# Kernel optimization log

Hardware: AMD Instinct MI355X
Metric: run time of the kernel (lower is better)

Reference implementation:

```python
import jax, jax.numpy as jnp
import numpy as np

N, E, C, H = 50000, 1_600_000, 128, 128
NUM_GRAPHS = 64


def setup_inputs() -> dict:
    key = jax.random.key(0)
    ks = jax.random.split(key, 9)
    x = jax.random.normal(ks[0], (N, C), dtype=jnp.float32)
    edge_index = jax.random.randint(ks[1], (2, E), 0, N, dtype=jnp.int64)
    edge_index_neg = jax.random.randint(ks[2], (2, E), 0, N, dtype=jnp.int64)
    batch = jnp.sort(jax.random.randint(ks[3], (N,), 0, NUM_GRAPHS, dtype=jnp.int64))
    W1 = jax.random.normal(ks[4], (C, H), dtype=jnp.float32) * 0.05
    b1 = jnp.zeros((H,), dtype=jnp.float32)
    W2 = jax.random.normal(ks[5], (H, H), dtype=jnp.float32) * 0.05
    b2 = jnp.zeros((H,), dtype=jnp.float32)
    We = jax.random.normal(ks[6], (2 * H, 1), dtype=jnp.float32) * 0.05
    be = jnp.zeros((1,), dtype=jnp.float32)
    return {"x": x, "edge_index": edge_index, "edge_index_neg": edge_index_neg,
            "batch": batch, "W1": W1, "b1": b1, "W2": W2, "b2": b2,
            "We": We, "be": be}


def reference(x, edge_index, edge_index_neg, batch, W1, b1, W2, b2, We, be):
    # x_enc: Linear -> ReLU -> Linear, then outer ReLU activation (eval mode, dropout=0)
    h = jax.nn.relu(jnp.dot(x, W1) + b1)          # [N, H]
    h = jax.nn.relu(jnp.dot(h, W2) + b2)          # [N, H]
    # p_e_x(cat([q, k])) == q @ We[:H] + k @ We[H:] + be  (avoids materializing cat)
    hdim = W1.shape[1]
    Wq, Wk = We[:hdim], We[hdim:]                  # [H,1] each

    def edge_score(ei):
        q = h[ei[0]]                               # [E, H] gather
        k = h[ei[1]]                               # [E, H] gather
        return jnp.dot(q, Wq) + jnp.dot(k, Wk) + be  # [E, 1]

    e_pred_pos = edge_score(edge_index)
    e_pred_neg = edge_score(edge_index_neg)
    return (e_pred_pos, e_pred_neg, edge_index_neg)
```

## Files before the change

kernel.cpp:

```cpp
#include <hip/hip_runtime.h>

#define CDIM 128
#define HDIM 128
#define LIM  40960

typedef short bf16x8 __attribute__((ext_vector_type(8)));
typedef float f32x16 __attribute__((ext_vector_type(16)));

static __device__ __forceinline__ short f2bf(float f) {
    union { float f; unsigned u; } v; v.f = f;
    unsigned r = v.u + 0x7FFFu + ((v.u >> 16) & 1u);
    return (short)(r >> 16);
}
static __device__ __forceinline__ unsigned pack2(float a, float b) {
    return (unsigned)(unsigned short)f2bf(a) | ((unsigned)(unsigned short)f2bf(b) << 16);
}

__global__ __launch_bounds__(256) void prep_kernel(
    const float* __restrict__ W1, const float* __restrict__ W2,
    short* __restrict__ wf1, short* __restrict__ wf2)
{
    int id = blockIdx.x * 256 + threadIdx.x;
    const float* src = (id < 16384) ? W1 : W2;
    short* dst = (id < 16384) ? wf1 : wf2;
    int rem = id & 16383;
    int j  = rem & 7;
    int l  = (rem >> 3) & 63;
    int ks = (rem >> 9) & 7;
    int ct = rem >> 12;
    int k = ks * 16 + (l >> 5) * 8 + j;
    int n = ct * 32 + (l & 31);
    dst[rem] = f2bf(src[k * HDIM + n]);
}

__global__ __launch_bounds__(256, 2) void node_mfma(
    const float* __restrict__ x,
    const short* __restrict__ wf1, const float* __restrict__ b1,
    const short* __restrict__ wf2, const float* __restrict__ b2,
    const float* __restrict__ We,
    unsigned* __restrict__ tab, int N)
{
    __shared__ __align__(16) short wfA[2][16384];
    __shared__ __align__(16) float cv[512];

    const int tid = threadIdx.x;
    const int w   = tid >> 6;
    const int l   = tid & 63;
    const int col = l & 31;
    const int hi  = l >> 5;
    const int node = blockIdx.x * 128 + w * 32 + col;

#pragma unroll
    for (int t = 0; t < 16; t++) {
        int c = (t * 4 + w) * 64;
        const uint4* src = (c < 2048) ? ((const uint4*)wf1 + c)
                                      : ((const uint4*)wf2 + (c - 2048));
        __builtin_amdgcn_global_load_lds(
            (const __attribute__((address_space(1))) void*)(src + l),
            (__attribute__((address_space(3))) void*)((char*)wfA + (size_t)c * 16),
            16, 0, 0);
    }
    for (int i = tid; i < 512; i += 256)
        cv[i] = (i < 128) ? b1[i] : (i < 256) ? b2[i - 128] : We[i - 256];
    __syncthreads();

    const f32x16 zz = {0.f,0.f,0.f,0.f,0.f,0.f,0.f,0.f,0.f,0.f,0.f,0.f,0.f,0.f,0.f,0.f};

    const int nclamp = (node < N) ? node : (N - 1);
    const float* xb = &x[(size_t)nclamp * CDIM + hi * 8];
    f32x16 acc[4];
#pragma unroll
    for (int ct = 0; ct < 4; ct++) acc[ct] = zz;

#pragma unroll
    for (int ks = 0; ks < 8; ks++) {
        float4 v0 = *(const float4*)(xb + ks * 16);
        float4 v1 = *(const float4*)(xb + ks * 16 + 4);
        bf16x8 a;
        a[0] = f2bf(v0.x); a[1] = f2bf(v0.y); a[2] = f2bf(v0.z); a[3] = f2bf(v0.w);
        a[4] = f2bf(v1.x); a[5] = f2bf(v1.y); a[6] = f2bf(v1.z); a[7] = f2bf(v1.w);
#pragma unroll
        for (int ct = 0; ct < 4; ct++) {
            bf16x8 wfrag = *(const bf16x8*)&wfA[0][((ct * 8 + ks) * 64 + l) * 8];
            acc[ct] = __builtin_amdgcn_mfma_f32_32x32x16_bf16(wfrag, a, acc[ct], 0, 0, 0);
        }
    }

    unsigned P[4][4][2], Q[4][4][2];
#pragma unroll
    for (int ct = 0; ct < 4; ct++) {
#pragma unroll
        for (int g = 0; g < 4; g++) {
            float4 bv = *(const float4*)&cv[32 * ct + 8 * g + 4 * hi];
            float h0 = fmaxf(acc[ct][4 * g + 0] + bv.x, 0.f);
            float h1v = fmaxf(acc[ct][4 * g + 1] + bv.y, 0.f);
            float h2v = fmaxf(acc[ct][4 * g + 2] + bv.z, 0.f);
            float h3v = fmaxf(acc[ct][4 * g + 3] + bv.w, 0.f);
            P[ct][g][0] = pack2(h0, h1v);
            P[ct][g][1] = pack2(h2v, h3v);
        }
    }
#pragma unroll
    for (int ct = 0; ct < 4; ct++)
#pragma unroll
        for (int g = 0; g < 4; g++)
#pragma unroll
            for (int p = 0; p < 2; p++)
                Q[ct][g][p] = (unsigned)__shfl_xor((int)P[ct][g][p], 32, 64);

    f32x16 acc2[4];
#pragma unroll
    for (int ct = 0; ct < 4; ct++) acc2[ct] = zz;

#pragma unroll
    for (int ks2 = 0; ks2 < 8; ks2++) {
        const int c  = ks2 >> 1;
        const int s2 = (ks2 & 1) * 2;
        union { bf16x8 v; unsigned u[4]; } bb;
        bb.u[0] = hi ? Q[c][s2 + 1][0] : P[c][s2][0];
        bb.u[1] = hi ? Q[c][s2 + 1][1] : P[c][s2][1];
        bb.u[2] = hi ? P[c][s2 + 1][0] : Q[c][s2][0];
        bb.u[3] = hi ? P[c][s2 + 1][1] : Q[c][s2][1];
#pragma unroll
        for (int ct = 0; ct < 4; ct++) {
            bf16x8 wfrag = *(const bf16x8*)&wfA[1][((ct * 8 + ks2) * 64 + l) * 8];
            acc2[ct] = __builtin_amdgcn_mfma_f32_32x32x16_bf16(wfrag, bb.v, acc2[ct], 0, 0, 0);
        }
    }

    float pq = 0.f, pk = 0.f;
#pragma unroll
    for (int ct = 0; ct < 4; ct++) {
#pragma unroll
        for (int g = 0; g < 4; g++) {
            float4 b2v = *(const float4*)&cv[128 + 32 * ct + 8 * g + 4 * hi];
            float4 wqv = *(const float4*)&cv[256 + 32 * ct + 8 * g + 4 * hi];
            float4 wkv = *(const float4*)&cv[384 + 32 * ct + 8 * g + 4 * hi];
            const float* b2a = (const float*)&b2v;
            const float* wqa = (const float*)&wqv;
            const float* wka = (const float*)&wkv;
#pragma unroll
            for (int i = 0; i < 4; i++) {
                float hv = fmaxf(acc2[ct][4 * g + i] + b2a[i], 0.f);
                pq = fmaf(hv, wqa[i], pq);
                pk = fmaf(hv, wka[i], pk);
            }
        }
    }
    pq += __shfl_xor(pq, 32, 64);
    pk += __shfl_xor(pk, 32, 64);
    if (hi == 0 && node < N) tab[node] = pack2(pq, pk);
}

__global__ __launch_bounds__(1024) void edge_kernel(
    const int* __restrict__ eip, const int* __restrict__ ein,
    const unsigned* __restrict__ tab, const float* __restrict__ be_p,
    float* __restrict__ out, int E)
{
    __shared__ __align__(16) unsigned lt[LIM];
    const int tid = threadIdx.x;
    const int wv = tid >> 6, ln = tid & 63;

    const uint4* tg4 = (const uint4*)tab;
#pragma unroll
    for (int t = 0; t < LIM / 4 / 1024; t++) {
        int c = (t * 16 + wv) * 64;
        __builtin_amdgcn_global_load_lds(
            (const __attribute__((address_space(1))) void*)(tg4 + c + ln),
            (__attribute__((address_space(3))) void*)((char*)lt + (size_t)c * 16),
            16, 0, 0);
    }
    __builtin_amdgcn_sched_barrier(0);

    const int U = E >> 2;
    const int chunk = (U + gridDim.x - 1) / gridDim.x;
    const int ustart = blockIdx.x * chunk;
    const int uend = min(U, ustart + chunk);

    const int4* eip4 = (const int4*)eip;
    const int4* ein4 = (const int4*)ein;
    float4* out4 = (float4*)out;

    const int u0 = ustart + tid, u1 = u0 + 1024;
    const bool v0 = u0 < uend, v1 = u1 < uend;
    int4 ns0 = {0,0,0,0}, nd0 = {0,0,0,0}, ns1 = {0,0,0,0}, nd1 = {0,0,0,0};
    if (v0) {
        ns0 = ein4[u0]; nd0 = ein4[U + u0];
        out4[2 * U + u0] = make_float4((float)ns0.x, (float)ns0.y, (float)ns0.z, (float)ns0.w);
        out4[3 * U + u0] = make_float4((float)nd0.x, (float)nd0.y, (float)nd0.z, (float)nd0.w);
    }
    if (v1) {
        ns1 = ein4[u1]; nd1 = ein4[U + u1];
        out4[2 * U + u1] = make_float4((float)ns1.x, (float)ns1.y, (float)ns1.z, (float)ns1.w);
        out4[3 * U + u1] = make_float4((float)nd1.x, (float)nd1.y, (float)nd1.z, (float)nd1.w);
    }
    __syncthreads();

    const float be = be_p[0];
#define GATHER(i) ((i) < LIM ? lt[i] : tab[i])
#define SCORE(us, ud) (__uint_as_float((us) << 16) + __uint_as_float((ud) & 0xFFFF0000u) + be)

    if (v0) {
        int4 ps = eip4[u0], pd = eip4[U + u0];
        unsigned a0 = GATHER(ps.x), a1 = GATHER(ps.y), a2 = GATHER(ps.z), a3 = GATHER(ps.w);
        unsigned b0 = GATHER(pd.x), b1 = GATHER(pd.y), b2 = GATHER(pd.z), b3 = GATHER(pd.w);
        unsigned c0 = GATHER(ns0.x), c1 = GATHER(ns0.y), c2 = GATHER(ns0.z), c3 = GATHER(ns0.w);
        unsigned d0 = GATHER(nd0.x), d1 = GATHER(nd0.y), d2 = GATHER(nd0.z), d3 = GATHER(nd0.w);
        out4[u0]     = make_float4(SCORE(a0,b0), SCORE(a1,b1), SCORE(a2,b2), SCORE(a3,b3));
        out4[U + u0] = make_float4(SCORE(c0,d0), SCORE(c1,d1), SCORE(c2,d2), SCORE(c3,d3));
    }
    if (v1) {
        int4 ps = eip4[u1], pd = eip4[U + u1];
        unsigned a0 = GATHER(ps.x), a1 = GATHER(ps.y), a2 = GATHER(ps.z), a3 = GATHER(ps.w);
        unsigned b0 = GATHER(pd.x), b1 = GATHER(pd.y), b2 = GATHER(pd.z), b3 = GATHER(pd.w);
        unsigned c0 = GATHER(ns1.x), c1 = GATHER(ns1.y), c2 = GATHER(ns1.z), c3 = GATHER(ns1.w);
        unsigned d0 = GATHER(nd1.x), d1 = GATHER(nd1.y), d2 = GATHER(nd1.z), d3 = GATHER(nd1.w);
        out4[u1]     = make_float4(SCORE(a0,b0), SCORE(a1,b1), SCORE(a2,b2), SCORE(a3,b3));
        out4[U + u1] = make_float4(SCORE(c0,d0), SCORE(c1,d1), SCORE(c2,d2), SCORE(c3,d3));
    }
#undef GATHER
#undef SCORE
}

extern "C" void kernel_launch(void* const* d_in, const int* in_sizes, int n_in,
                              void* d_out, int out_size, void* d_ws, size_t ws_size,
                              hipStream_t stream) {
    const float* x   = (const float*)d_in[0];
    const int*   eip = (const int*)d_in[1];
    const int*   ein = (const int*)d_in[2];
    const float* W1  = (const float*)d_in[4];
    const float* b1  = (const float*)d_in[5];
    const float* W2  = (const float*)d_in[6];
    const float* b2  = (const float*)d_in[7];
    const float* We  = (const float*)d_in[8];
    const float* be  = (const float*)d_in[9];

    const int N = in_sizes[0] / CDIM;
    const int E = in_sizes[1] / 2;

    char* ws = (char*)d_ws;
    unsigned* tab = (unsigned*)ws;
    short*    wf1 = (short*)(ws + 200704);
    short*    wf2 = (short*)(ws + 200704 + 32768);

    prep_kernel<<<128, 256, 0, stream>>>(W1, W2, wf1, wf2);
    node_mfma<<<(N + 127) / 128, 256, 0, stream>>>(x, wf1, b1, wf2, b2, We, tab, N);
    edge_kernel<<<256, 1024, 0, stream>>>(eip, ein, tab, be, (float*)d_out, E);
}
```

Measured before the change: 32.69 us.

## Move negative edge-index copy into node kernel and enlarge node tiles

The float cast of edge_index_neg into the output moves out of the edge kernel and into the node MLP kernel. That kernel now runs as a fixed grid of 256 blocks with 512 threads and 256 nodes per block; blocks past N only do the copy. The x loads are hoisted ahead of the weight-staging barrier, and the prep kernel now reads W1/W2 coalesced and scatters its writes. The edge kernel issues its index loads earlier. The aim is to spread the copy bandwidth over the compute-bound node phase and shorten the gather kernel, at the cost of more registers per thread in the node kernel.

```diff
diff --git a/kernel.cpp b/kernel.cpp
--- a/kernel.cpp
+++ b/kernel.cpp
@@ -2,6 +2,7 @@
 
 #define CDIM 128
 #define HDIM 128
+#define TILE 256
 #define LIM  40960
 
 typedef short bf16x8 __attribute__((ext_vector_type(8)));
@@ -24,21 +25,20 @@
     const float* src = (id < 16384) ? W1 : W2;
     short* dst = (id < 16384) ? wf1 : wf2;
     int rem = id & 16383;
-    int j  = rem & 7;
-    int l  = (rem >> 3) & 63;
-    int ks = (rem >> 9) & 7;
-    int ct = rem >> 12;
-    int k = ks * 16 + (l >> 5) * 8 + j;
-    int n = ct * 32 + (l & 31);
-    dst[rem] = f2bf(src[k * HDIM + n]);
-}
-
-__global__ __launch_bounds__(256, 2) void node_mfma(
+    int k = rem >> 7, n = rem & 127;
+    int ks = k >> 4, j = k & 7;
+    int l  = (n & 31) + 32 * ((k >> 3) & 1);
+    int ct = n >> 5;
+    dst[((ct * 8 + ks) * 64 + l) * 8 + j] = f2bf(src[rem]);
+}
+
+__global__ __launch_bounds__(512) void node_mfma(
     const float* __restrict__ x,
     const short* __restrict__ wf1, const float* __restrict__ b1,
     const short* __restrict__ wf2, const float* __restrict__ b2,
     const float* __restrict__ We,
-    unsigned* __restrict__ tab, int N)
+    const int* __restrict__ ein,
+    unsigned* __restrict__ tab, float* __restrict__ out, int N, int E)
 {
     __shared__ __align__(16) short wfA[2][16384];
     __shared__ __align__(16) float cv[512];
@@ -48,108 +48,127 @@
     const int l   = tid & 63;
     const int col = l & 31;
     const int hi  = l >> 5;
-    const int node = blockIdx.x * 128 + w * 32 + col;
-
-#pragma unroll
-    for (int t = 0; t < 16; t++) {
-        int c = (t * 4 + w) * 64;
-        const uint4* src = (c < 2048) ? ((const uint4*)wf1 + c)
-                                      : ((const uint4*)wf2 + (c - 2048));
-        __builtin_amdgcn_global_load_lds(
-            (const __attribute__((address_space(1))) void*)(src + l),
-            (__attribute__((address_space(3))) void*)((char*)wfA + (size_t)c * 16),
-            16, 0, 0);
-    }
-    for (int i = tid; i < 512; i += 256)
-        cv[i] = (i < 128) ? b1[i] : (i < 256) ? b2[i - 128] : We[i - 256];
-    __syncthreads();
-
-    const f32x16 zz = {0.f,0.f,0.f,0.f,0.f,0.f,0.f,0.f,0.f,0.f,0.f,0.f,0.f,0.f,0.f,0.f};
-
-    const int nclamp = (node < N) ? node : (N - 1);
-    const float* xb = &x[(size_t)nclamp * CDIM + hi * 8];
-    f32x16 acc[4];
-#pragma unroll
-    for (int ct = 0; ct < 4; ct++) acc[ct] = zz;
-
-#pragma unroll
-    for (int ks = 0; ks < 8; ks++) {
-        float4 v0 = *(const float4*)(xb + ks * 16);
-        float4 v1 = *(const float4*)(xb + ks * 16 + 4);
-        bf16x8 a;
-        a[0] = f2bf(v0.x); a[1] = f2bf(v0.y); a[2] = f2bf(v0.z); a[3] = f2bf(v0.w);
-        a[4] = f2bf(v1.x); a[5] = f2bf(v1.y); a[6] = f2bf(v1.z); a[7] = f2bf(v1.w);
+    const int node = blockIdx.x * TILE + w * 32 + col;
+    const bool nodeblk = (blockIdx.x * TILE) < N;
+
+    if (nodeblk) {
+#pragma unroll
+        for (int t = 0; t < 8; t++) {
+            int c = (t * 8 + w) * 64;
+            const uint4* src = (c < 2048) ? ((const uint4*)wf1 + c)
+                                          : ((const uint4*)wf2 + (c - 2048));
+            __builtin_amdgcn_global_load_lds(
+                (const __attribute__((address_space(1))) void*)(src + l),
+                (__attribute__((address_space(3))) void*)((char*)wfA + (size_t)c * 16),
+                16, 0, 0);
+        }
+        cv[tid] = (tid < 128) ? b1[tid] : (tid < 256) ? b2[tid - 128] : We[tid - 256];
+
+        const int nclamp = (node < N) ? node : (N - 1);
+        const float* xb = &x[(size_t)nclamp * CDIM + hi * 8];
+        bf16x8 af[8];
+#pragma unroll
+        for (int ks = 0; ks < 8; ks++) {
+            float4 v0 = *(const float4*)(xb + ks * 16);
+            float4 v1 = *(const float4*)(xb + ks * 16 + 4);
+            af[ks][0] = f2bf(v0.x); af[ks][1] = f2bf(v0.y);
+            af[ks][2] = f2bf(v0.z); af[ks][3] = f2bf(v0.w);
+            af[ks][4] = f2bf(v1.x); af[ks][5] = f2bf(v1.y);
+            af[ks][6] = f2bf(v1.z); af[ks][7] = f2bf(v1.w);
+        }
+        __syncthreads();
+
+        const f32x16 zz = {0.f,0.f,0.f,0.f,0.f,0.f,0.f,0.f,0.f,0.f,0.f,0.f,0.f,0.f,0.f,0.f};
+
+        f32x16 acc[4];
+#pragma unroll
+        for (int ct = 0; ct < 4; ct++) acc[ct] = zz;
+#pragma unroll
+        for (int ks = 0; ks < 8; ks++) {
+#pragma unroll
+            for (int ct = 0; ct < 4; ct++) {
+                bf16x8 wfrag = *(const bf16x8*)&wfA[0][((ct * 8 + ks) * 64 + l) * 8];
+                acc[ct] = __builtin_amdgcn_mfma_f32_32x32x16_bf16(wfrag, af[ks], acc[ct], 0, 0, 0);
+            }
+        }
+
+        unsigned P[4][4][2], Q[4][4][2];
 #pragma unroll
         for (int ct = 0; ct < 4; ct++) {
-            bf16x8 wfrag = *(const bf16x8*)&wfA[0][((ct * 8 + ks) * 64 + l) * 8];
-            acc[ct] = __builtin_amdgcn_mfma_f32_32x32x16_bf16(wfrag, a, acc[ct], 0, 0, 0);
-        }
-    }
-
-    unsigned P[4][4][2], Q[4][4][2];
-#pragma unroll
-    for (int ct = 0; ct < 4; ct++) {
-#pragma unroll
-        for (int g = 0; g < 4; g++) {
-            float4 bv = *(const float4*)&cv[32 * ct + 8 * g + 4 * hi];
-            float h0 = fmaxf(acc[ct][4 * g + 0] + bv.x, 0.f);
-            float h1v = fmaxf(acc[ct][4 * g + 1] + bv.y, 0.f);
-            float h2v = fmaxf(acc[ct][4 * g + 2] + bv.z, 0.f);
-            float h3v = fmaxf(acc[ct][4 * g + 3] + bv.w, 0.f);
-            P[ct][g][0] = pack2(h0, h1v);
-            P[ct][g][1] = pack2(h2v, h3v);
-        }
-    }
-#pragma unroll
-    for (int ct = 0; ct < 4; ct++)
-#pragma unroll
-        for (int g = 0; g < 4; g++)
-#pragma unroll
-            for (int p = 0; p < 2; p++)
-                Q[ct][g][p] = (unsigned)__shfl_xor((int)P[ct][g][p], 32, 64);
-
-    f32x16 acc2[4];
-#pragma unroll
-    for (int ct = 0; ct < 4; ct++) acc2[ct] = zz;
-
-#pragma unroll
-    for (int ks2 = 0; ks2 < 8; ks2++) {
-        const int c  = ks2 >> 1;
-        const int s2 = (ks2 & 1) * 2;
-        union { bf16x8 v; unsigned u[4]; } bb;
-        bb.u[0] = hi ? Q[c][s2 + 1][0] : P[c][s2][0];
-        bb.u[1] = hi ? Q[c][s2 + 1][1] : P[c][s2][1];
-        bb.u[2] = hi ? P[c][s2 + 1][0] : Q[c][s2][0];
-        bb.u[3] = hi ? P[c][s2 + 1][1] : Q[c][s2][1];
+#pragma unroll
+            for (int g = 0; g < 4; g++) {
+                float4 bv = *(const float4*)&cv[32 * ct + 8 * g + 4 * hi];
+                float h0  = fmaxf(acc[ct][4 * g + 0] + bv.x, 0.f);
+                float h1v = fmaxf(acc[ct][4 * g + 1] + bv.y, 0.f);
+                float h2v = fmaxf(acc[ct][4 * g + 2] + bv.z, 0.f);
+                float h3v = fmaxf(acc[ct][4 * g + 3] + bv.w, 0.f);
+                P[ct][g][0] = pack2(h0, h1v);
+                P[ct][g][1] = pack2(h2v, h3v);
+            }
+        }
+#pragma unroll
+        for (int ct = 0; ct < 4; ct++)
+#pragma unroll
+            for (int g = 0; g < 4; g++)
+#pragma unroll
+                for (int p = 0; p < 2; p++)
+                    Q[ct][g][p] = (unsigned)__shfl_xor((int)P[ct][g][p], 32, 64);
+
+        f32x16 acc2[4];
+#pragma unroll
+        for (int ct = 0; ct < 4; ct++) acc2[ct] = zz;
+#pragma unroll
+        for (int ks2 = 0; ks2 < 8; ks2++) {
+            const int c  = ks2 >> 1;
+            const int s2 = (ks2 & 1) * 2;
+            union { bf16x8 v; unsigned u[4]; } bb;
+            bb.u[0] = hi ? Q[c][s2 + 1][0] : P[c][s2][0];
+            bb.u[1] = hi ? Q[c][s2 + 1][1] : P[c][s2][1];
+            bb.u[2] = hi ? P[c][s2 + 1][0] : Q[c][s2][0];
+            bb.u[3] = hi ? P[c][s2 + 1][1] : Q[c][s2][1];
+#pragma unroll
+            for (int ct = 0; ct < 4; ct++) {
+                bf16x8 wfrag = *(const bf16x8*)&wfA[1][((ct * 8 + ks2) * 64 + l) * 8];
+                acc2[ct] = __builtin_amdgcn_mfma_f32_32x32x16_bf16(wfrag, bb.v, acc2[ct], 0, 0, 0);
+            }
+        }
+
+        float pq = 0.f, pk = 0.f;
 #pragma unroll
         for (int ct = 0; ct < 4; ct++) {
-            bf16x8 wfrag = *(const bf16x8*)&wfA[1][((ct * 8 + ks2) * 64 + l) * 8];
-            acc2[ct] = __builtin_amdgcn_mfma_f32_32x32x16_bf16(wfrag, bb.v, acc2[ct], 0, 0, 0);
-        }
-    }
-
-    float pq = 0.f, pk = 0.f;
-#pragma unroll
-    for (int ct = 0; ct < 4; ct++) {
-#pragma unroll
-        for (int g = 0; g < 4; g++) {
-            float4 b2v = *(const float4*)&cv[128 + 32 * ct + 8 * g + 4 * hi];
-            float4 wqv = *(const float4*)&cv[256 + 32 * ct + 8 * g + 4 * hi];
-            float4 wkv = *(const float4*)&cv[384 + 32 * ct + 8 * g + 4 * hi];
-            const float* b2a = (const float*)&b2v;
-            const float* wqa = (const float*)&wqv;
-            const float* wka = (const float*)&wkv;
-#pragma unroll
-            for (int i = 0; i < 4; i++) {
-                float hv = fmaxf(acc2[ct][4 * g + i] + b2a[i], 0.f);
-                pq = fmaf(hv, wqa[i], pq);
-                pk = fmaf(hv, wka[i], pk);
-            }
-        }
-    }
-    pq += __shfl_xor(pq, 32, 64);
-    pk += __shfl_xor(pk, 32, 64);
-    if (hi == 0 && node < N) tab[node] = pack2(pq, pk);
+#pragma unroll
+            for (int g = 0; g < 4; g++) {
+                float4 b2v = *(const float4*)&cv[128 + 32 * ct + 8 * g + 4 * hi];
+                float4 wqv = *(const float4*)&cv[256 + 32 * ct + 8 * g + 4 * hi];
+                float4 wkv = *(const float4*)&cv[384 + 32 * ct + 8 * g + 4 * hi];
+                const float* b2a = (const float*)&b2v;
+                const float* wqa = (const float*)&wqv;
+                const float* wka = (const float*)&wkv;
+#pragma unroll
+                for (int i = 0; i < 4; i++) {
+                    float hv = fmaxf(acc2[ct][4 * g + i] + b2a[i], 0.f);
+                    pq = fmaf(hv, wqa[i], pq);
+                    pk = fmaf(hv, wka[i], pk);
+                }
+            }
+        }
+        pq += __shfl_xor(pq, 32, 64);
+        pk += __shfl_xor(pk, 32, 64);
+        if (hi == 0 && node < N) tab[node] = pack2(pq, pk);
+    }
+
+    {
+        const int castU = (E * 2) >> 2;
+        const int chunk = (castU + gridDim.x - 1) / gridDim.x;
+        const int base = blockIdx.x * chunk;
+        const int lim = min(castU, base + chunk);
+        const int4* ein4 = (const int4*)ein;
+        float4* o4 = (float4*)out + (E >> 1);
+        for (int i = base + tid; i < lim; i += 512) {
+            int4 v = ein4[i];
+            o4[i] = make_float4((float)v.x, (float)v.y, (float)v.z, (float)v.w);
+        }
+    }
 }
 
 __global__ __launch_bounds__(1024) void edge_kernel(
@@ -183,39 +202,35 @@
 
     const int u0 = ustart + tid, u1 = u0 + 1024;
     const bool v0 = u0 < uend, v1 = u1 < uend;
+
     int4 ns0 = {0,0,0,0}, nd0 = {0,0,0,0}, ns1 = {0,0,0,0}, nd1 = {0,0,0,0};
+    int4 ps0 = {0,0,0,0}, pd0 = {0,0,0,0};
     if (v0) {
         ns0 = ein4[u0]; nd0 = ein4[U + u0];
-        out4[2 * U + u0] = make_float4((float)ns0.x, (float)ns0.y, (float)ns0.z, (float)ns0.w);
-        out4[3 * U + u0] = make_float4((float)nd0.x, (float)nd0.y, (float)nd0.z, (float)nd0.w);
-    }
-    if (v1) {
-        ns1 = ein4[u1]; nd1 = ein4[U + u1];
-        out4[2 * U + u1] = make_float4((float)ns1.x, (float)ns1.y, (float)ns1.z, (float)ns1.w);
-        out4[3 * U + u1] = make_float4((float)nd1.x, (float)nd1.y, (float)nd1.z, (float)nd1.w);
-    }
+        ps0 = eip4[u0]; pd0 = eip4[U + u0];
+    }
+    if (v1) { ns1 = ein4[u1]; nd1 = ein4[U + u1]; }
+
     __syncthreads();
 
     const float be = be_p[0];
 #define GATHER(i) ((i) < LIM ? lt[i] : tab[i])
 #define SCORE(us, ud) (__uint_as_float((us) << 16) + __uint_as_float((ud) & 0xFFFF0000u) + be)
-
     if (v0) {
-        int4 ps = eip4[u0], pd = eip4[U + u0];
-        unsigned a0 = GATHER(ps.x), a1 = GATHER(ps.y), a2 = GATHER(ps.z), a3 = GATHER(ps.w);
-        unsigned b0 = GATHER(pd.x), b1 = GATHER(pd.y), b2 = GATHER(pd.z), b3 = GATHER(pd.w);
+        unsigned a0 = GATHER(ps0.x), a1 = GATHER(ps0.y), a2 = GATHER(ps0.z), a3 = GATHER(ps0.w);
+        unsigned b0 = GATHER(pd0.x), b1 = GATHER(pd0.y), b2 = GATHER(pd0.z), b3 = GATHER(pd0.w);
+        out4[u0] = make_float4(SCORE(a0,b0), SCORE(a1,b1), SCORE(a2,b2), SCORE(a3,b3));
         unsigned c0 = GATHER(ns0.x), c1 = GATHER(ns0.y), c2 = GATHER(ns0.z), c3 = GATHER(ns0.w);
         unsigned d0 = GATHER(nd0.x), d1 = GATHER(nd0.y), d2 = GATHER(nd0.z), d3 = GATHER(nd0.w);
-        out4[u0]     = make_float4(SCORE(a0,b0), SCORE(a1,b1), SCORE(a2,b2), SCORE(a3,b3));
         out4[U + u0] = make_float4(SCORE(c0,d0), SCORE(c1,d1), SCORE(c2,d2), SCORE(c3,d3));
     }
     if (v1) {
-        int4 ps = eip4[u1], pd = eip4[U + u1];
-        unsigned a0 = GATHER(ps.x), a1 = GATHER(ps.y), a2 = GATHER(ps.z), a3 = GATHER(ps.w);
-        unsigned b0 = GATHER(pd.x), b1 = GATHER(pd.y), b2 = GATHER(pd.z), b3 = GATHER(pd.w);
+        int4 ps1 = eip4[u1], pd1 = eip4[U + u1];
+        unsigned a0 = GATHER(ps1.x), a1 = GATHER(ps1.y), a2 = GATHER(ps1.z), a3 = GATHER(ps1.w);
+        unsigned b0 = GATHER(pd1.x), b1 = GATHER(pd1.y), b2 = GATHER(pd1.z), b3 = GATHER(pd1.w);
+        out4[u1] = make_float4(SCORE(a0,b0), SCORE(a1,b1), SCORE(a2,b2), SCORE(a3,b3));
         unsigned c0 = GATHER(ns1.x), c1 = GATHER(ns1.y), c2 = GATHER(ns1.z), c3 = GATHER(ns1.w);
         unsigned d0 = GATHER(nd1.x), d1 = GATHER(nd1.y), d2 = GATHER(nd1.z), d3 = GATHER(nd1.w);
-        out4[u1]     = make_float4(SCORE(a0,b0), SCORE(a1,b1), SCORE(a2,b2), SCORE(a3,b3));
         out4[U + u1] = make_float4(SCORE(c0,d0), SCORE(c1,d1), SCORE(c2,d2), SCORE(c3,d3));
     }
 #undef GATHER
@@ -244,6 +259,7 @@
     short*    wf2 = (short*)(ws + 200704 + 32768);
 
     prep_kernel<<<128, 256, 0, stream>>>(W1, W2, wf1, wf2);
-    node_mfma<<<(N + 127) / 128, 256, 0, stream>>>(x, wf1, b1, wf2, b2, We, tab, N);
+    node_mfma<<<256, 512, 0, stream>>>(x, wf1, b1, wf2, b2, We, ein, tab,
+                                       (float*)d_out, N, E);
     edge_kernel<<<256, 1024, 0, stream>>>(eip, ein, tab, be, (float*)d_out, E);
 }
```

Result: slower. 33.55 us (+2.6%).
